# Optimization experiments

Measured on AMD Instinct MI355X. Metric: run time of the kernel, lower is better.

Reference implementation:

```python
import jax, jax.numpy as jnp
import numpy as np

V, BLOCK, L, H, E, B, T = 1024, 2048, 4, 8, 512, 4, 2048
D = E // H  # head dim = 64

def setup_inputs() -> dict:
    key = jax.random.key(0)
    ks = jax.random.split(key, 8)
    s = 0.02
    return {
        "idx": jax.random.randint(ks[0], (B, T), 0, V),
        "wte": jax.random.normal(ks[1], (V, E), jnp.float32) * s,
        "wpe": jax.random.normal(ks[2], (BLOCK, E), jnp.float32) * s,
        "ln1_w": jnp.ones((L, E), jnp.float32),
        "ln1_b": jnp.zeros((L, E), jnp.float32),
        "attn_w": jax.random.normal(ks[3], (L, 3 * E, E), jnp.float32) * s,
        "attn_b": jnp.zeros((L, 3 * E), jnp.float32),
        "proj_w": jax.random.normal(ks[4], (L, E, E), jnp.float32) * s,
        "proj_b": jnp.zeros((L, E), jnp.float32),
        "ln2_w": jnp.ones((L, E), jnp.float32),
        "ln2_b": jnp.zeros((L, E), jnp.float32),
        "fc_w": jax.random.normal(ks[5], (L, 4 * E, E), jnp.float32) * s,
        "fc_b": jnp.zeros((L, 4 * E), jnp.float32),
        "fc2_w": jax.random.normal(ks[6], (L, E, 4 * E), jnp.float32) * s,
        "fc2_b": jnp.zeros((L, E), jnp.float32),
        "lnf_w": jnp.ones((E,), jnp.float32),
        "lnf_b": jnp.zeros((E,), jnp.float32),
    }

def layer_norm(x, w, b, eps=1e-5):
    mu = jnp.mean(x, axis=-1, keepdims=True)
    var = jnp.var(x, axis=-1, keepdims=True)
    return (x - mu) * jax.lax.rsqrt(var + eps) * w + b

def reference(idx, wte, wpe, ln1_w, ln1_b, attn_w, attn_b, proj_w, proj_b,
              ln2_w, ln2_b, fc_w, fc_b, fc2_w, fc2_b, lnf_w, lnf_b):
    b, t = idx.shape
    x = wte[idx] + wpe[:t]  # (B,T,E)
    causal = jnp.tril(jnp.ones((t, t), bool))
    scale = 1.0 / np.sqrt(D)

    def block(x, p):
        l1w, l1b, aw, ab, pw, pb, l2w, l2b, fw, fb, f2w, f2b = p
        h = layer_norm(x, l1w, l1b)
        qkv = h @ aw.T + ab  # (B,T,3E)
        q, k, v = jnp.split(qkv, 3, axis=-1)
        q = q.reshape(b, t, H, D)
        k = k.reshape(b, t, H, D)
        v = v.reshape(b, t, H, D)
        att = jnp.einsum('bqhd,bkhd->bhqk', q, k) * scale
        att = jnp.where(causal, att, -jnp.inf)
        att = jax.nn.softmax(att, axis=-1)
        y = jnp.einsum('bhqk,bkhd->bqhd', att, v).reshape(b, t, E)
        x = x + y @ pw.T + pb
        h2 = layer_norm(x, l2w, l2b)
        h2 = jax.nn.gelu(h2 @ fw.T + fb, approximate=False)
        x = x + h2 @ f2w.T + f2b
        return x, None

    params = (ln1_w, ln1_b, attn_w, attn_b, proj_w, proj_b,
              ln2_w, ln2_b, fc_w, fc_b, fc2_w, fc2_b)
    x, _ = jax.lax.scan(block, x, params)
    x = layer_norm(x, lnf_w, lnf_b)
    logits = x @ wte.T  # tied lm_head
    return logits
```

## Files before the change

### kernel.cpp

```cpp
#include <hip/hip_runtime.h>
#include <hip/hip_bf16.h>
#include <math.h>

#define B_ 4
#define T_ 2048
#define E_ 512
#define H_ 8
#define D_ 64
#define L_ 4
#define V_ 1024
#define NROWS (B_*T_)
#define KBLK 64
#define KVPAD 72
#define PPAD 72

typedef __hip_bfloat16 bf16;
typedef __attribute__((ext_vector_type(8))) short bf16x8;
typedef __attribute__((ext_vector_type(4))) float f32x4;

__device__ __forceinline__ short f2bf_s(float f) {
    union { bf16 h; short s; } t; t.h = __float2bfloat16(f); return t.s;
}

__device__ __forceinline__ void gload_lds16(const bf16* g, bf16* l) {
    __builtin_amdgcn_global_load_lds((const __attribute__((address_space(1))) void*)g,
                                     (__attribute__((address_space(3))) void*)l, 16, 0, 0);
}

__global__ void f2bf_all(const float* __restrict__ s0, const float* __restrict__ s1,
                         const float* __restrict__ s2, const float* __restrict__ s3,
                         const float* __restrict__ s4, bf16* __restrict__ dst) {
    size_t gi = (size_t)blockIdx.x * 1024 + threadIdx.x * 4;
    const float* src; size_t off;
    if (blockIdx.x < 3072)       { src = s0; off = gi; }
    else if (blockIdx.x < 4096)  { src = s1; off = gi - (size_t)3072 * 1024; }
    else if (blockIdx.x < 8192)  { src = s2; off = gi - (size_t)4096 * 1024; }
    else if (blockIdx.x < 12288) { src = s3; off = gi - (size_t)8192 * 1024; }
    else                         { src = s4; off = gi - (size_t)12288 * 1024; }
    float4 v = *(const float4*)(src + off);
    union { bf16 h[4]; uint2 u; } t;
    t.h[0] = __float2bfloat16(v.x); t.h[1] = __float2bfloat16(v.y);
    t.h[2] = __float2bfloat16(v.z); t.h[3] = __float2bfloat16(v.w);
    *(uint2*)(dst + gi) = t.u;
}

__global__ void embed_kernel(const int* __restrict__ idx, const float* __restrict__ wte,
                             const float* __restrict__ wpe, float* __restrict__ x) {
    int i = (blockIdx.x * blockDim.x + threadIdx.x) * 4;
    int row = i >> 9;
    int e = i & (E_ - 1);
    int t = row & (T_ - 1);
    int id = idx[row];
    float4 a = *(const float4*)(wte + (size_t)id * E_ + e);
    float4 p = *(const float4*)(wpe + (size_t)t * E_ + e);
    a.x += p.x; a.y += p.y; a.z += p.z; a.w += p.w;
    *(float4*)(x + i) = a;
}

__global__ __launch_bounds__(512) void layernorm_kernel(const float* __restrict__ x,
                                 const float* __restrict__ w, const float* __restrict__ b,
                                 bf16* __restrict__ out) {
    int wid = threadIdx.x >> 6, lane = threadIdx.x & 63;
    int row = blockIdx.x * 8 + wid;
    const float* xr = x + (size_t)row * E_ + lane * 8;
    float4 a0 = *(const float4*)xr;
    float4 a1 = *(const float4*)(xr + 4);
    float s = (a0.x + a0.y) + (a0.z + a0.w) + (a1.x + a1.y) + (a1.z + a1.w);
    float q = a0.x*a0.x + a0.y*a0.y + a0.z*a0.z + a0.w*a0.w
            + a1.x*a1.x + a1.y*a1.y + a1.z*a1.z + a1.w*a1.w;
    #pragma unroll
    for (int st = 1; st < 64; st <<= 1) { s += __shfl_xor(s, st); q += __shfl_xor(q, st); }
    float mean = s * (1.0f / E_);
    float var = q * (1.0f / E_) - mean * mean;
    float rstd = rsqrtf(var + 1e-5f);
    float4 w0 = *(const float4*)(w + lane * 8), w1 = *(const float4*)(w + lane * 8 + 4);
    float4 b0 = *(const float4*)(b + lane * 8), b1 = *(const float4*)(b + lane * 8 + 4);
    union { bf16 h[8]; uint4 u; } o;
    o.h[0] = __float2bfloat16((a0.x - mean) * rstd * w0.x + b0.x);
    o.h[1] = __float2bfloat16((a0.y - mean) * rstd * w0.y + b0.y);
    o.h[2] = __float2bfloat16((a0.z - mean) * rstd * w0.z + b0.z);
    o.h[3] = __float2bfloat16((a0.w - mean) * rstd * w0.w + b0.w);
    o.h[4] = __float2bfloat16((a1.x - mean) * rstd * w1.x + b1.x);
    o.h[5] = __float2bfloat16((a1.y - mean) * rstd * w1.y + b1.y);
    o.h[6] = __float2bfloat16((a1.z - mean) * rstd * w1.z + b1.z);
    o.h[7] = __float2bfloat16((a1.w - mean) * rstd * w1.w + b1.w);
    *(uint4*)(out + (size_t)row * E_ + lane * 8) = o.u;
}

template<int ACT, int OMODE, bool BIAS, bool QKV>
__global__ __launch_bounds__(256) void gemm_mfma(const bf16* __restrict__ A, const bf16* __restrict__ W,
        const float* __restrict__ bias, float* __restrict__ Cf, bf16* __restrict__ Cb,
        bf16* __restrict__ Vt, int M, int N, int K) {
    __shared__ __align__(16) bf16 As[128][32];
    __shared__ __align__(16) bf16 Bs[128][32];
    int tid = threadIdx.x;
    int lane = tid & 63, wid = tid >> 6;
    int wm = (wid >> 1) * 64, wn = (wid & 1) * 64;
    int m0 = blockIdx.y * 128, n0 = blockIdx.x * 128;

    int srow = wid * 32 + (lane >> 2);
    int scol = (lane & 3) * 8;
    const bf16* ga = A + (size_t)(m0 + srow) * K + scol;
    const bf16* gb = W + (size_t)(n0 + srow) * K + scol;
    int fr = lane & 15, fk = (lane >> 4) * 8;

    f32x4 acc[4][4];
    #pragma unroll
    for (int i = 0; i < 4; ++i)
        #pragma unroll
        for (int j = 0; j < 4; ++j) acc[i][j] = (f32x4){0.f, 0.f, 0.f, 0.f};

    for (int k0 = 0; k0 < K; k0 += 32) {
        gload_lds16(ga,          &As[wid * 32][0]);
        gload_lds16(ga + 16 * K, &As[wid * 32 + 16][0]);
        gload_lds16(gb,          &Bs[wid * 32][0]);
        gload_lds16(gb + 16 * K, &Bs[wid * 32 + 16][0]);
        ga += 32; gb += 32;
        __syncthreads();
        bf16x8 af[4], bff[4];
        #pragma unroll
        for (int i = 0; i < 4; ++i) af[i]  = *(const bf16x8*)&As[wm + i * 16 + fr][fk];
        #pragma unroll
        for (int j = 0; j < 4; ++j) bff[j] = *(const bf16x8*)&Bs[wn + j * 16 + fr][fk];
        #pragma unroll
        for (int i = 0; i < 4; ++i)
            #pragma unroll
            for (int j = 0; j < 4; ++j)
                acc[i][j] = __builtin_amdgcn_mfma_f32_16x16x32_bf16(af[i], bff[j], acc[i][j], 0, 0, 0);
        __syncthreads();
    }

    int orow = m0 + wm + (lane >> 4) * 4;
    int ocol = n0 + wn + (lane & 15);

    if (QKV && n0 >= 2 * E_) {
        #pragma unroll
        for (int i = 0; i < 4; ++i) {
            int rowb = orow + i * 16;
            int bb = rowb >> 11;
            int t0 = rowb & (T_ - 1);
            #pragma unroll
            for (int j = 0; j < 4; ++j) {
                int col = ocol + j * 16;
                int dg = col - 2 * E_;
                int hh = dg >> 6, dd = dg & 63;
                float bv = BIAS ? bias[col] : 0.0f;
                union { bf16 h[4]; short4 s4; } pk;
                #pragma unroll
                for (int r = 0; r < 4; ++r)
                    pk.h[r] = __float2bfloat16(acc[i][j][r] + bv);
                *(short4*)&Vt[(((size_t)bb * H_ + hh) * D_ + dd) * T_ + t0] = pk.s4;
            }
        }
        return;
    }

    #pragma unroll
    for (int i = 0; i < 4; ++i) {
        #pragma unroll
        for (int j = 0; j < 4; ++j) {
            #pragma unroll
            for (int r = 0; r < 4; ++r) {
                int row = orow + i * 16 + r;
                int col = ocol + j * 16;
                float v = acc[i][j][r];
                if (BIAS) v += bias[col];
                if (ACT == 1) v = 0.5f * v * (1.0f + erff(v * 0.70710678118654752f));
                if (QKV) {
                    if (col < E_) v *= 0.125f;
                    Cb[(size_t)row * (2 * E_) + col] = __float2bfloat16(v);
                } else {
                    size_t off = (size_t)row * N + col;
                    if (OMODE == 0) Cf[off] = v;
                    else if (OMODE == 1) Cb[off] = __float2bfloat16(v);
                    else Cf[off] += v;
                }
            }
        }
    }
}

template<bool DOMASK>
__device__ __forceinline__ void attn_tile(
        const short (&Ks)[KBLK][KVPAD], const short (&VsT)[D_][KVPAD],
        short (*Psw)[PPAD], const bf16x8 (&qf)[2],
        float& m_run, float& l_run, f32x4 (&accO)[4],
        int fr, int fg, int k0, int qrow) {
    f32x4 st[4];
    __builtin_amdgcn_s_setprio(1);
    #pragma unroll
    for (int j = 0; j < 4; ++j) {
        f32x4 a = (f32x4){0.f, 0.f, 0.f, 0.f};
        #pragma unroll
        for (int kk = 0; kk < 2; ++kk) {
            bf16x8 kf = *(const bf16x8*)&Ks[j * 16 + fr][kk * 32 + fg * 8];
            a = __builtin_amdgcn_mfma_f32_16x16x32_bf16(kf, qf[kk], a, 0, 0, 0);
        }
        st[j] = a;
    }
    __builtin_amdgcn_s_setprio(0);
    float mx = -INFINITY;
    #pragma unroll
    for (int j = 0; j < 4; ++j)
        #pragma unroll
        for (int r = 0; r < 4; ++r) {
            if (DOMASK && (k0 + j * 16 + fg * 4 + r > qrow)) st[j][r] = -INFINITY;
            mx = fmaxf(mx, st[j][r]);
        }
    mx = fmaxf(mx, __shfl_xor(mx, 16));
    mx = fmaxf(mx, __shfl_xor(mx, 32));
    if (!__all(mx <= m_run + 8.0f)) {
        float mnew = fmaxf(m_run, mx);
        float corr = __expf(m_run - mnew);
        l_run *= corr;
        #pragma unroll
        for (int r = 0; r < 4; ++r) {
            float cr = __shfl(corr, fg * 4 + r);
            #pragma unroll
            for (int n = 0; n < 4; ++n) accO[n][r] *= cr;
        }
        m_run = mnew;
    }
    float rl = 0.0f;
    #pragma unroll
    for (int j = 0; j < 4; ++j) {
        float p0 = __expf(st[j][0] - m_run), p1 = __expf(st[j][1] - m_run);
        float p2 = __expf(st[j][2] - m_run), p3 = __expf(st[j][3] - m_run);
        rl += (p0 + p1) + (p2 + p3);
        short4 pk;
        pk.x = f2bf_s(p0); pk.y = f2bf_s(p1); pk.z = f2bf_s(p2); pk.w = f2bf_s(p3);
        *(short4*)&Psw[fr][j * 16 + fg * 4] = pk;
    }
    rl += __shfl_xor(rl, 16);
    rl += __shfl_xor(rl, 32);
    l_run += rl;
    __builtin_amdgcn_s_setprio(1);
    bf16x8 pa[2];
    #pragma unroll
    for (int kk = 0; kk < 2; ++kk)
        pa[kk] = *(const bf16x8*)&Psw[fr][kk * 32 + fg * 8];
    #pragma unroll
    for (int n = 0; n < 4; ++n)
        #pragma unroll
        for (int kk = 0; kk < 2; ++kk) {
            bf16x8 vb = *(const bf16x8*)&VsT[n * 16 + fr][kk * 32 + fg * 8];
            accO[n] = __builtin_amdgcn_mfma_f32_16x16x32_bf16(pa[kk], vb, accO[n], 0, 0, 0);
        }
    __builtin_amdgcn_s_setprio(0);
}

__global__ __launch_bounds__(256, 4) void attn_mfma(const bf16* __restrict__ qk,
                                                    const bf16* __restrict__ vt,
                                                    bf16* __restrict__ y) {
    __shared__ __align__(16) short Ks[KBLK][KVPAD];
    __shared__ __align__(16) short VsT[D_][KVPAD];
    __shared__ __align__(16) short Ps[4][16][PPAD];
    const int qi = (gridDim.x - 1) - blockIdx.x;
    const int h = blockIdx.y, b = blockIdx.z;
    const int q0 = qi * 64;
    const int tid = threadIdx.x;
    const int lane = tid & 63, wid = tid >> 6;
    const int fr = lane & 15, fg = lane >> 4;
    const int qmin = q0 + wid * 16;
    const int qrow = qmin + fr;

    const int sr0 = tid >> 3;
    const int sc = (tid & 7) * 8;
    const bf16* kst = qk + (size_t)(b * T_ + sr0) * (2 * E_) + E_ + h * D_ + sc;
    const bf16* vst = vt + ((size_t)(b * H_ + h) * D_ + sr0) * T_ + sc;

    const bf16* qbase = qk + (size_t)(b * T_ + qrow) * (2 * E_) + h * D_;
    bf16x8 qf[2];
    #pragma unroll
    for (int kk = 0; kk < 2; ++kk)
        qf[kk] = *(const bf16x8*)(qbase + kk * 32 + fg * 8);

    float m_run = -INFINITY, l_run = 0.0f;
    f32x4 accO[4];
    #pragma unroll
    for (int n = 0; n < 4; ++n) accO[n] = (f32x4){0.f, 0.f, 0.f, 0.f};

    const int ntiles = qi + 1;

    {
        uint4 k0r = *(const uint4*)kst;
        uint4 k1r = *(const uint4*)(kst + 32 * (2 * E_));
        uint4 v0r = *(const uint4*)vst;
        uint4 v1r = *(const uint4*)(vst + 32 * T_);
        *(uint4*)&Ks[sr0][sc] = k0r;  *(uint4*)&Ks[sr0 + 32][sc] = k1r;
        *(uint4*)&VsT[sr0][sc] = v0r; *(uint4*)&VsT[sr0 + 32][sc] = v1r;
    }
    __syncthreads();

    for (int kt = 0; kt < ntiles; ++kt) {
        const bool have_next = (kt + 1 < ntiles);
        uint4 nk0, nk1, nv0, nv1;
        if (have_next) {
            const bf16* kn = kst + (size_t)(kt + 1) * KBLK * (2 * E_);
            const bf16* vn = vst + (kt + 1) * KBLK;
            nk0 = *(const uint4*)kn; nk1 = *(const uint4*)(kn + 32 * (2 * E_));
            nv0 = *(const uint4*)vn; nv1 = *(const uint4*)(vn + 32 * T_);
        }

        if (kt + 1 == ntiles)
            attn_tile<true >(Ks, VsT, Ps[wid], qf, m_run, l_run, accO, fr, fg, kt * KBLK, qrow);
        else
            attn_tile<false>(Ks, VsT, Ps[wid], qf, m_run, l_run, accO, fr, fg, kt * KBLK, qrow);

        __syncthreads();
        if (have_next) {
            *(uint4*)&Ks[sr0][sc] = nk0;  *(uint4*)&Ks[sr0 + 32][sc] = nk1;
            *(uint4*)&VsT[sr0][sc] = nv0; *(uint4*)&VsT[sr0 + 32][sc] = nv1;
            __syncthreads();
        }
    }

    float linv = 1.0f / l_run;
    #pragma unroll
    for (int r = 0; r < 4; ++r) {
        float lr = __shfl(linv, fg * 4 + r);
        int gq = qmin + fg * 4 + r;
        #pragma unroll
        for (int n = 0; n < 4; ++n)
            y[(size_t)(b * T_ + gq) * E_ + h * D_ + n * 16 + fr] =
                __float2bfloat16(accO[n][r] * lr);
    }
}

extern "C" void kernel_launch(void* const* d_in, const int* in_sizes, int n_in,
                              void* d_out, int out_size, void* d_ws, size_t ws_size,
                              hipStream_t stream) {
    const int*   idx    = (const int*)d_in[0];
    const float* wte    = (const float*)d_in[1];
    const float* wpe    = (const float*)d_in[2];
    const float* ln1_w  = (const float*)d_in[3];
    const float* ln1_b  = (const float*)d_in[4];
    const float* attn_w = (const float*)d_in[5];
    const float* attn_b = (const float*)d_in[6];
    const float* proj_w = (const float*)d_in[7];
    const float* proj_b = (const float*)d_in[8];
    const float* ln2_w  = (const float*)d_in[9];
    const float* ln2_b  = (const float*)d_in[10];
    const float* fc_w   = (const float*)d_in[11];
    const float* fc_b   = (const float*)d_in[12];
    const float* fc2_w  = (const float*)d_in[13];
    const float* fc2_b  = (const float*)d_in[14];
    const float* lnf_w  = (const float*)d_in[15];
    const float* lnf_b  = (const float*)d_in[16];
    float* out = (float*)d_out;

    float* x   = (float*)d_ws;
    bf16* hbf  = (bf16*)(x + (size_t)NROWS * E_);
    bf16* big  = hbf + (size_t)NROWS * E_;
    bf16* qkb  = big;
    bf16* vtb  = big + (size_t)NROWS * 2 * E_;
    bf16* wb   = big + (size_t)NROWS * 4 * E_;
    bf16* attn_wb = wb;
    bf16* proj_wb = attn_wb + (size_t)L_ * 3 * E_ * E_;
    bf16* fc_wb   = proj_wb + (size_t)L_ * E_ * E_;
    bf16* fc2_wb  = fc_wb   + (size_t)L_ * 4 * E_ * E_;
    bf16* wte_b   = fc2_wb  + (size_t)L_ * E_ * 4 * E_;

    f2bf_all<<<12800, 256, 0, stream>>>(attn_w, proj_w, fc_w, fc2_w, wte, wb);
    embed_kernel<<<NROWS * E_ / 1024, 256, 0, stream>>>(idx, wte, wpe, x);

    for (int l = 0; l < L_; ++l) {
        layernorm_kernel<<<NROWS / 8, 512, 0, stream>>>(x, ln1_w + l * E_, ln1_b + l * E_, hbf);
        gemm_mfma<0, 1, true, true><<<dim3(3 * E_ / 128, NROWS / 128), 256, 0, stream>>>(
            hbf, attn_wb + (size_t)l * 3 * E_ * E_, attn_b + l * 3 * E_, nullptr, qkb, vtb,
            NROWS, 3 * E_, E_);
        attn_mfma<<<dim3(T_ / 64, H_, B_), 256, 0, stream>>>(qkb, vtb, hbf);
        gemm_mfma<0, 2, true, false><<<dim3(E_ / 128, NROWS / 128), 256, 0, stream>>>(
            hbf, proj_wb + (size_t)l * E_ * E_, proj_b + l * E_, x, nullptr, nullptr,
            NROWS, E_, E_);
        layernorm_kernel<<<NROWS / 8, 512, 0, stream>>>(x, ln2_w + l * E_, ln2_b + l * E_, hbf);
        gemm_mfma<1, 1, true, false><<<dim3(4 * E_ / 128, NROWS / 128), 256, 0, stream>>>(
            hbf, fc_wb + (size_t)l * 4 * E_ * E_, fc_b + l * 4 * E_, nullptr, big, nullptr,
            NROWS, 4 * E_, E_);
        gemm_mfma<0, 2, true, false><<<dim3(E_ / 128, NROWS / 128), 256, 0, stream>>>(
            big, fc2_wb + (size_t)l * E_ * 4 * E_, fc2_b + l * E_, x, nullptr, nullptr,
            NROWS, E_, 4 * E_);
    }
    layernorm_kernel<<<NROWS / 8, 512, 0, stream>>>(x, lnf_w, lnf_b, hbf);
    gemm_mfma<0, 0, false, false><<<dim3(V_ / 128, NROWS / 128), 256, 0, stream>>>(
        hbf, wte_b, nullptr, out, nullptr, nullptr, NROWS, V_, E_);
}
```

Before: 980.1 us.

## Split long causal attention rows across two KV chunks with combine kernel

Query blocks in the second half of the sequence now process their KV tiles in two halves run by separate workgroups, each writing unnormalized partial outputs plus running max/sum. A new combine kernel merges the two partials with log-sum-exp rescaling. This aims to shorten the longest-running attention workgroups and improve load balance. In exchange it adds an extra launch, bf16 partial writes and reads, and early-exit blocks in the doubled grid.

```diff
diff --git a/kernel.cpp b/kernel.cpp
--- a/kernel.cpp
+++ b/kernel.cpp
@@ -13,6 +13,7 @@
 #define KBLK 64
 #define KVPAD 72
 #define PPAD 72
+#define SPLT 16
 
 typedef __hip_bfloat16 bf16;
 typedef __attribute__((ext_vector_type(8))) short bf16x8;
@@ -251,12 +252,21 @@
 
 __global__ __launch_bounds__(256, 4) void attn_mfma(const bf16* __restrict__ qk,
                                                     const bf16* __restrict__ vt,
-                                                    bf16* __restrict__ y) {
+                                                    bf16* __restrict__ y,
+                                                    bf16* __restrict__ opart,
+                                                    float2* __restrict__ mlb) {
     __shared__ __align__(16) short Ks[KBLK][KVPAD];
     __shared__ __align__(16) short VsT[D_][KVPAD];
     __shared__ __align__(16) short Ps[4][16][PPAD];
     const int qi = (gridDim.x - 1) - blockIdx.x;
-    const int h = blockIdx.y, b = blockIdx.z;
+    const int sp = blockIdx.y >> 3;
+    const int h = blockIdx.y & 7, b = blockIdx.z;
+    const int nt = qi + 1;
+    const bool split_mode = (qi >= SPLT);
+    if (!split_mode && sp == 1) return;
+    const int t0i = split_mode ? sp * SPLT : 0;
+    const int t1i = split_mode ? min(nt, t0i + SPLT) : nt;
+
     const int q0 = qi * 64;
     const int tid = threadIdx.x;
     const int lane = tid & 63, wid = tid >> 6;
@@ -280,20 +290,20 @@
     #pragma unroll
     for (int n = 0; n < 4; ++n) accO[n] = (f32x4){0.f, 0.f, 0.f, 0.f};
 
-    const int ntiles = qi + 1;
-
     {
-        uint4 k0r = *(const uint4*)kst;
-        uint4 k1r = *(const uint4*)(kst + 32 * (2 * E_));
-        uint4 v0r = *(const uint4*)vst;
-        uint4 v1r = *(const uint4*)(vst + 32 * T_);
+        const bf16* kp = kst + (size_t)t0i * KBLK * (2 * E_);
+        const bf16* vp = vst + t0i * KBLK;
+        uint4 k0r = *(const uint4*)kp;
+        uint4 k1r = *(const uint4*)(kp + 32 * (2 * E_));
+        uint4 v0r = *(const uint4*)vp;
+        uint4 v1r = *(const uint4*)(vp + 32 * T_);
         *(uint4*)&Ks[sr0][sc] = k0r;  *(uint4*)&Ks[sr0 + 32][sc] = k1r;
         *(uint4*)&VsT[sr0][sc] = v0r; *(uint4*)&VsT[sr0 + 32][sc] = v1r;
     }
     __syncthreads();
 
-    for (int kt = 0; kt < ntiles; ++kt) {
-        const bool have_next = (kt + 1 < ntiles);
+    for (int kt = t0i; kt < t1i; ++kt) {
+        const bool have_next = (kt + 1 < t1i);
         uint4 nk0, nk1, nv0, nv1;
         if (have_next) {
             const bf16* kn = kst + (size_t)(kt + 1) * KBLK * (2 * E_);
@@ -302,7 +312,7 @@
             nv0 = *(const uint4*)vn; nv1 = *(const uint4*)(vn + 32 * T_);
         }
 
-        if (kt + 1 == ntiles)
+        if (kt == nt - 1)
             attn_tile<true >(Ks, VsT, Ps[wid], qf, m_run, l_run, accO, fr, fg, kt * KBLK, qrow);
         else
             attn_tile<false>(Ks, VsT, Ps[wid], qf, m_run, l_run, accO, fr, fg, kt * KBLK, qrow);
@@ -315,16 +325,42 @@
         }
     }
 
-    float linv = 1.0f / l_run;
-    #pragma unroll
-    for (int r = 0; r < 4; ++r) {
-        float lr = __shfl(linv, fg * 4 + r);
-        int gq = qmin + fg * 4 + r;
-        #pragma unroll
-        for (int n = 0; n < 4; ++n)
-            y[(size_t)(b * T_ + gq) * E_ + h * D_ + n * 16 + fr] =
-                __float2bfloat16(accO[n][r] * lr);
-    }
+    if (split_mode) {
+        size_t rbase = (size_t)sp * 32768 + (size_t)b * 8192 + (size_t)h * 1024 + (qmin - 1024);
+        if (lane < 16) mlb[rbase + lane] = make_float2(m_run, l_run);
+        #pragma unroll
+        for (int r = 0; r < 4; ++r) {
+            #pragma unroll
+            for (int n = 0; n < 4; ++n)
+                opart[(rbase + fg * 4 + r) * D_ + n * 16 + fr] = __float2bfloat16(accO[n][r]);
+        }
+    } else {
+        float linv = 1.0f / l_run;
+        #pragma unroll
+        for (int r = 0; r < 4; ++r) {
+            float lr = __shfl(linv, fg * 4 + r);
+            int gq = qmin + fg * 4 + r;
+            #pragma unroll
+            for (int n = 0; n < 4; ++n)
+                y[(size_t)(b * T_ + gq) * E_ + h * D_ + n * 16 + fr] =
+                    __float2bfloat16(accO[n][r] * lr);
+        }
+    }
+}
+
+__global__ __launch_bounds__(512) void attn_combine(const bf16* __restrict__ opart,
+        const float2* __restrict__ mlb, bf16* __restrict__ y) {
+    int lane = threadIdx.x & 63, wid = threadIdx.x >> 6;
+    int row = blockIdx.x * 8 + wid;
+    int b = row >> 13, h = (row >> 10) & 7, trel = row & 1023;
+    float2 s0 = mlb[row];
+    float2 s1 = mlb[32768 + row];
+    float mm = fmaxf(s0.x, s1.x);
+    float w0 = __expf(s0.x - mm), w1 = __expf(s1.x - mm);
+    float l = w0 * s0.y + w1 * s1.y;
+    float o = w0 * __bfloat162float(opart[(size_t)row * D_ + lane])
+            + w1 * __bfloat162float(opart[((size_t)32768 + row) * D_ + lane]);
+    y[(size_t)(b * T_ + 1024 + trel) * E_ + h * D_ + lane] = __float2bfloat16(o / l);
 }
 
 extern "C" void kernel_launch(void* const* d_in, const int* in_sizes, int n_in,
@@ -354,12 +390,14 @@
     bf16* big  = hbf + (size_t)NROWS * E_;
     bf16* qkb  = big;
     bf16* vtb  = big + (size_t)NROWS * 2 * E_;
+    bf16* opart = big + (size_t)NROWS * 3 * E_;
     bf16* wb   = big + (size_t)NROWS * 4 * E_;
     bf16* attn_wb = wb;
     bf16* proj_wb = attn_wb + (size_t)L_ * 3 * E_ * E_;
     bf16* fc_wb   = proj_wb + (size_t)L_ * E_ * E_;
     bf16* fc2_wb  = fc_wb   + (size_t)L_ * 4 * E_ * E_;
     bf16* wte_b   = fc2_wb  + (size_t)L_ * E_ * 4 * E_;
+    float2* mlb   = (float2*)(wte_b + (size_t)V_ * E_);
 
     f2bf_all<<<12800, 256, 0, stream>>>(attn_w, proj_w, fc_w, fc2_w, wte, wb);
     embed_kernel<<<NROWS * E_ / 1024, 256, 0, stream>>>(idx, wte, wpe, x);
@@ -369,7 +407,8 @@
         gemm_mfma<0, 1, true, true><<<dim3(3 * E_ / 128, NROWS / 128), 256, 0, stream>>>(
             hbf, attn_wb + (size_t)l * 3 * E_ * E_, attn_b + l * 3 * E_, nullptr, qkb, vtb,
             NROWS, 3 * E_, E_);
-        attn_mfma<<<dim3(T_ / 64, H_, B_), 256, 0, stream>>>(qkb, vtb, hbf);
+        attn_mfma<<<dim3(T_ / 64, H_ * 2, B_), 256, 0, stream>>>(qkb, vtb, hbf, opart, mlb);
+        attn_combine<<<32768 / 8, 512, 0, stream>>>(opart, mlb, hbf);
         gemm_mfma<0, 2, true, false><<<dim3(E_ / 128, NROWS / 128), 256, 0, stream>>>(
             hbf, proj_wb + (size_t)l * E_ * E_, proj_b + l * E_, x, nullptr, nullptr,
             NROWS, E_, E_);
```

After: 1.008 ms. 1.03x slower.

## Double-buffer GEMM LDS tiles and pass attention probabilities through lane shuffles

Applied to the files above, without the earlier changes.

The GEMM main loop now uses two LDS buffers for A and B. The next K-slice's global-to-LDS loads are issued before the MFMA work on the current slice, and one barrier per iteration is dropped, so load latency can overlap compute. In attention, the bf16 probability tile is packed in registers and redistributed into MFMA A-operand layout with cross-lane shuffles instead of a per-wave LDS round trip, which also removes the Ps shared buffer. The costs are doubled GEMM shared memory and sixteen shuffles per tile in attention. Correctness depends on the barrier waiting for the asynchronous LDS loads.

```diff
diff --git a/kernel.cpp b/kernel.cpp
--- a/kernel.cpp
+++ b/kernel.cpp
@@ -12,7 +12,6 @@
 #define NROWS (B_*T_)
 #define KBLK 64
 #define KVPAD 72
-#define PPAD 72
 
 typedef __hip_bfloat16 bf16;
 typedef __attribute__((ext_vector_type(8))) short bf16x8;
@@ -20,6 +19,10 @@
 
 __device__ __forceinline__ short f2bf_s(float f) {
     union { bf16 h; short s; } t; t.h = __float2bfloat16(f); return t.s;
+}
+__device__ __forceinline__ unsigned int pack2bf(float a, float b) {
+    return (unsigned int)(unsigned short)f2bf_s(a) |
+           ((unsigned int)(unsigned short)f2bf_s(b) << 16);
 }
 
 __device__ __forceinline__ void gload_lds16(const bf16* g, bf16* l) {
@@ -91,8 +94,8 @@
 __global__ __launch_bounds__(256) void gemm_mfma(const bf16* __restrict__ A, const bf16* __restrict__ W,
         const float* __restrict__ bias, float* __restrict__ Cf, bf16* __restrict__ Cb,
         bf16* __restrict__ Vt, int M, int N, int K) {
-    __shared__ __align__(16) bf16 As[128][32];
-    __shared__ __align__(16) bf16 Bs[128][32];
+    __shared__ __align__(16) bf16 As[2][128][32];
+    __shared__ __align__(16) bf16 Bs[2][128][32];
     int tid = threadIdx.x;
     int lane = tid & 63, wid = tid >> 6;
     int wm = (wid >> 1) * 64, wn = (wid & 1) * 64;
@@ -110,18 +113,28 @@
         #pragma unroll
         for (int j = 0; j < 4; ++j) acc[i][j] = (f32x4){0.f, 0.f, 0.f, 0.f};
 
-    for (int k0 = 0; k0 < K; k0 += 32) {
-        gload_lds16(ga,          &As[wid * 32][0]);
-        gload_lds16(ga + 16 * K, &As[wid * 32 + 16][0]);
-        gload_lds16(gb,          &Bs[wid * 32][0]);
-        gload_lds16(gb + 16 * K, &Bs[wid * 32 + 16][0]);
-        ga += 32; gb += 32;
-        __syncthreads();
+    gload_lds16(ga,          &As[0][wid * 32][0]);
+    gload_lds16(ga + 16 * K, &As[0][wid * 32 + 16][0]);
+    gload_lds16(gb,          &Bs[0][wid * 32][0]);
+    gload_lds16(gb + 16 * K, &Bs[0][wid * 32 + 16][0]);
+    __syncthreads();
+
+    const int nst = K >> 5;
+    for (int t = 0; t < nst; ++t) {
+        const int cur = t & 1;
+        if (t + 1 < nst) {
+            const bf16* ga2 = ga + (t + 1) * 32;
+            const bf16* gb2 = gb + (t + 1) * 32;
+            gload_lds16(ga2,          &As[cur ^ 1][wid * 32][0]);
+            gload_lds16(ga2 + 16 * K, &As[cur ^ 1][wid * 32 + 16][0]);
+            gload_lds16(gb2,          &Bs[cur ^ 1][wid * 32][0]);
+            gload_lds16(gb2 + 16 * K, &Bs[cur ^ 1][wid * 32 + 16][0]);
+        }
         bf16x8 af[4], bff[4];
         #pragma unroll
-        for (int i = 0; i < 4; ++i) af[i]  = *(const bf16x8*)&As[wm + i * 16 + fr][fk];
-        #pragma unroll
-        for (int j = 0; j < 4; ++j) bff[j] = *(const bf16x8*)&Bs[wn + j * 16 + fr][fk];
+        for (int i = 0; i < 4; ++i) af[i]  = *(const bf16x8*)&As[cur][wm + i * 16 + fr][fk];
+        #pragma unroll
+        for (int j = 0; j < 4; ++j) bff[j] = *(const bf16x8*)&Bs[cur][wn + j * 16 + fr][fk];
         #pragma unroll
         for (int i = 0; i < 4; ++i)
             #pragma unroll
@@ -183,7 +196,7 @@
 template<bool DOMASK>
 __device__ __forceinline__ void attn_tile(
         const short (&Ks)[KBLK][KVPAD], const short (&VsT)[D_][KVPAD],
-        short (*Psw)[PPAD], const bf16x8 (&qf)[2],
+        const bf16x8 (&qf)[2],
         float& m_run, float& l_run, f32x4 (&accO)[4],
         int fr, int fg, int k0, int qrow) {
     f32x4 st[4];
@@ -221,24 +234,37 @@
         }
         m_run = mnew;
     }
+    unsigned int dw[4][2];
     float rl = 0.0f;
     #pragma unroll
     for (int j = 0; j < 4; ++j) {
         float p0 = __expf(st[j][0] - m_run), p1 = __expf(st[j][1] - m_run);
         float p2 = __expf(st[j][2] - m_run), p3 = __expf(st[j][3] - m_run);
         rl += (p0 + p1) + (p2 + p3);
-        short4 pk;
-        pk.x = f2bf_s(p0); pk.y = f2bf_s(p1); pk.z = f2bf_s(p2); pk.w = f2bf_s(p3);
-        *(short4*)&Psw[fr][j * 16 + fg * 4] = pk;
+        dw[j][0] = pack2bf(p0, p1);
+        dw[j][1] = pack2bf(p2, p3);
     }
     rl += __shfl_xor(rl, 16);
     rl += __shfl_xor(rl, 32);
     l_run += rl;
+    const int laneA = ((fg & 1) << 5) + fr;
+    const int laneB = laneA + 16;
+    const bool selhi = (fg & 2) != 0;
+    bf16x8 pa[2];
+    #pragma unroll
+    for (int kk = 0; kk < 2; ++kk) {
+        unsigned int a0 = __shfl(dw[2 * kk][0], laneA), a1 = __shfl(dw[2 * kk + 1][0], laneA);
+        unsigned int b0 = __shfl(dw[2 * kk][1], laneA), b1 = __shfl(dw[2 * kk + 1][1], laneA);
+        unsigned int c0 = __shfl(dw[2 * kk][0], laneB), c1 = __shfl(dw[2 * kk + 1][0], laneB);
+        unsigned int d0 = __shfl(dw[2 * kk][1], laneB), d1 = __shfl(dw[2 * kk + 1][1], laneB);
+        union { unsigned int u[4]; bf16x8 v; } t;
+        t.u[0] = selhi ? a1 : a0;
+        t.u[1] = selhi ? b1 : b0;
+        t.u[2] = selhi ? c1 : c0;
+        t.u[3] = selhi ? d1 : d0;
+        pa[kk] = t.v;
+    }
     __builtin_amdgcn_s_setprio(1);
-    bf16x8 pa[2];
-    #pragma unroll
-    for (int kk = 0; kk < 2; ++kk)
-        pa[kk] = *(const bf16x8*)&Psw[fr][kk * 32 + fg * 8];
     #pragma unroll
     for (int n = 0; n < 4; ++n)
         #pragma unroll
@@ -254,7 +280,6 @@
                                                     bf16* __restrict__ y) {
     __shared__ __align__(16) short Ks[KBLK][KVPAD];
     __shared__ __align__(16) short VsT[D_][KVPAD];
-    __shared__ __align__(16) short Ps[4][16][PPAD];
     const int qi = (gridDim.x - 1) - blockIdx.x;
     const int h = blockIdx.y, b = blockIdx.z;
     const int q0 = qi * 64;
@@ -303,9 +328,9 @@
         }
 
         if (kt + 1 == ntiles)
-            attn_tile<true >(Ks, VsT, Ps[wid], qf, m_run, l_run, accO, fr, fg, kt * KBLK, qrow);
+            attn_tile<true >(Ks, VsT, qf, m_run, l_run, accO, fr, fg, kt * KBLK, qrow);
         else
-            attn_tile<false>(Ks, VsT, Ps[wid], qf, m_run, l_run, accO, fr, fg, kt * KBLK, qrow);
+            attn_tile<false>(Ks, VsT, qf, m_run, l_run, accO, fr, fg, kt * KBLK, qrow);
 
         __syncthreads();
         if (have_next) {
```

After: 996.9 us. No clear change (+1.7%).
